# Optimization experiments

Measured on AMD Instinct MI355X. Metric: run time of the kernel, lower is better.

The kernel has to match this reference:

```python
import jax, jax.numpy as jnp
import numpy as np

SCALING = 2.0  # alpha / r = 128 / 64


def setup_inputs() -> dict:
    key = jax.random.key(0)
    k1, k2, k3, k4, k5 = jax.random.split(key, 5)
    B, S, DIN, DOUT, R = 4, 2048, 4096, 4096, 64
    x = jax.random.normal(k1, (B, S, DIN), dtype=jnp.float32)
    # int8 quantized weight codes in [-127, 127] (stored as int32 for portability)
    qweight = jax.random.randint(k2, (DOUT, DIN), -127, 128, dtype=jnp.int32)
    # per-output-row absmax dequant scale (already divided by 127)
    scale = jax.random.uniform(k3, (DOUT, 1), dtype=jnp.float32, minval=0.005, maxval=0.02)
    lora_A = jax.random.normal(k4, (R, DIN), dtype=jnp.float32) * 0.02
    lora_B = jax.random.normal(k5, (DOUT, R), dtype=jnp.float32) * 0.02
    return {"x": x, "qweight": qweight, "scale": scale, "lora_A": lora_A, "lora_B": lora_B}


def reference(x, qweight, scale, lora_A, lora_B):
    # inline int8 dequant: w[o,i] = code[o,i] * scale[o]
    w = qweight.astype(x.dtype) * scale  # [DOUT, DIN]
    base = jnp.einsum('bsi,oi->bso', x, w)
    # low-rank LoRA path: (x @ A^T) @ B^T, scaled
    xa = jnp.einsum('bsi,ri->bsr', x, lora_A)       # [B,S,R]
    lora = jnp.einsum('bsr,or->bso', xa, lora_B)    # [B,S,DOUT]
    return base + SCALING * lora
```

## Files before the change

### kernel.cpp

```cpp
#include <hip/hip_runtime.h>
#include <hip/hip_bf16.h>
#include <stdint.h>


typedef __bf16 bf16x8 __attribute__((ext_vector_type(8)));
typedef float f32x4 __attribute__((ext_vector_type(4)));
typedef int i32x4 __attribute__((ext_vector_type(4)));

#define DIN   4096
#define DOUT  4096
#define MTOT  8192
#define RNK   64
#define NT    64

__device__ inline void gload_lds16(const void* g, void* l) {
  __builtin_amdgcn_global_load_lds((const __attribute__((address_space(1))) void*)g,
                                   (__attribute__((address_space(3))) void*)l,
                                   16, 0, 0);
}

__global__ __launch_bounds__(256) void quant_x_kernel(const float* __restrict__ x,
                                                      signed char* __restrict__ Xi8,
                                                      float* __restrict__ tstep) {
  const int row = blockIdx.x, t = threadIdx.x;
  const float4* xr = (const float4*)(x + (size_t)row * DIN);
  float4 v[4];
  float m = 0.f;
#pragma unroll
  for (int s = 0; s < 4; ++s) {
    v[s] = xr[t + s * 256];
    m = fmaxf(m, fmaxf(fmaxf(fabsf(v[s].x), fabsf(v[s].y)),
                       fmaxf(fabsf(v[s].z), fabsf(v[s].w))));
  }
#pragma unroll
  for (int off = 32; off > 0; off >>= 1) m = fmaxf(m, __shfl_xor(m, off));
  __shared__ float wm[4];
  if ((t & 63) == 0) wm[t >> 6] = m;
  __syncthreads();
  m = fmaxf(fmaxf(wm[0], wm[1]), fmaxf(wm[2], wm[3]));
  m = fmaxf(m, 1e-30f);
  const float rs = 127.0f / m;
  int* orow = (int*)(Xi8 + (size_t)row * DIN);
#pragma unroll
  for (int s = 0; s < 4; ++s) {
    float e[4] = {v[s].x, v[s].y, v[s].z, v[s].w};
    union { signed char c[4]; int i; } p;
#pragma unroll
    for (int j = 0; j < 4; ++j) {
      int q = __float2int_rn(e[j] * rs);
      q = q > 127 ? 127 : (q < -127 ? -127 : q);
      p.c[j] = (signed char)q;
    }
    orow[t + s * 256] = p.i;
  }
  if (t == 0) tstep[row] = m * (1.0f / 127.0f);
}

__global__ void cvt_w_kernel(const int* __restrict__ q, signed char* __restrict__ Wi8) {
  int i = blockIdx.x * blockDim.x + threadIdx.x;
  int4 v = ((const int4*)q)[i];
  union { signed char c[4]; int i; } p;
  p.c[0] = (signed char)v.x; p.c[1] = (signed char)v.y;
  p.c[2] = (signed char)v.z; p.c[3] = (signed char)v.w;
  ((int*)Wi8)[i] = p.i;
}

__global__ __launch_bounds__(256) void cvt_ab_kernel(const float* __restrict__ A,
                                                     const float* __restrict__ B,
                                                     signed char* __restrict__ Ai8,
                                                     float* __restrict__ astep,
                                                     __bf16* __restrict__ Blt) {
  const int t = threadIdx.x;
  if (blockIdx.x < 64) {
    const int row = blockIdx.x;
    const float4* ar = (const float4*)(A + (size_t)row * DIN);
    float4 v[4];
    float m = 0.f;
#pragma unroll
    for (int s = 0; s < 4; ++s) {
      v[s] = ar[t + s * 256];
      m = fmaxf(m, fmaxf(fmaxf(fabsf(v[s].x), fabsf(v[s].y)),
                         fmaxf(fabsf(v[s].z), fabsf(v[s].w))));
    }
#pragma unroll
    for (int off = 32; off > 0; off >>= 1) m = fmaxf(m, __shfl_xor(m, off));
    __shared__ float wm[4];
    if ((t & 63) == 0) wm[t >> 6] = m;
    __syncthreads();
    m = fmaxf(fmaxf(wm[0], wm[1]), fmaxf(wm[2], wm[3]));
    m = fmaxf(m, 1e-30f);
    const float rs = 127.0f / m;
    int* orow = (int*)(Ai8 + (size_t)row * DIN);
#pragma unroll
    for (int s = 0; s < 4; ++s) {
      float e[4] = {v[s].x, v[s].y, v[s].z, v[s].w};
      union { signed char c[4]; int i; } p;
#pragma unroll
      for (int j = 0; j < 4; ++j) {
        int q = __float2int_rn(e[j] * rs);
        q = q > 127 ? 127 : (q < -127 ? -127 : q);
        p.c[j] = (signed char)q;
      }
      orow[t + s * 256] = p.i;
    }
    if (t == 0) astep[row] = m * (1.0f / 127.0f);
  } else {
    int i = (blockIdx.x - 64) * 256 + t;
    float4 v = ((const float4*)B)[i];
    union { __bf16 h[4]; uint64_t u; } p;
    p.h[0] = (__bf16)(2.0f * v.x); p.h[1] = (__bf16)(2.0f * v.y);
    p.h[2] = (__bf16)(2.0f * v.z); p.h[3] = (__bf16)(2.0f * v.w);
    ((uint64_t*)Blt)[i] = p.u;
  }
}

__global__ __launch_bounds__(128) void lora_xa_kernel(const signed char* __restrict__ Xi8,
                                                      const float* __restrict__ tstep,
                                                      const signed char* __restrict__ Ai8,
                                                      const float* __restrict__ astep,
                                                      __bf16* __restrict__ xa) {
  int wid = threadIdx.x >> 6, lane = threadIdx.x & 63;
  int rowbase = blockIdx.x * 32 + wid * 16;
  i32x4 acc[4] = {};
  const signed char* xrow = Xi8 + (size_t)(rowbase + (lane & 15)) * DIN + (lane >> 4) * 16;
  const signed char* ab = Ai8 + (size_t)(lane & 15) * DIN + (lane >> 4) * 16;
  for (int k0 = 0; k0 < DIN; k0 += 64) {
    i32x4 af = *(const i32x4*)(xrow + k0);
#pragma unroll
    for (int ni = 0; ni < 4; ++ni) {
      i32x4 bv = *(const i32x4*)(ab + (size_t)ni * 16 * DIN + k0);
      acc[ni] = __builtin_amdgcn_mfma_i32_16x16x64_i8(af, bv, acc[ni], 0, 0, 0);
    }
  }
  f32x4 tm = *(const f32x4*)&tstep[rowbase + (lane >> 4) * 4];
#pragma unroll
  for (int ni = 0; ni < 4; ++ni) {
    const int col = ni * 16 + (lane & 15);
    const float as = astep[col];
#pragma unroll
    for (int j = 0; j < 4; ++j) {
      int row = rowbase + (lane >> 4) * 4 + j;
      xa[(size_t)row * RNK + col] = (__bf16)((float)acc[ni][j] * tm[j] * as);
    }
  }
}

__global__ __launch_bounds__(512, 1) void gemm_i8_kernel(const signed char* __restrict__ Xi8,
                                                         const signed char* __restrict__ Wi8,
                                                         const float* __restrict__ scale,
                                                         const float* __restrict__ tstep,
                                                         const __bf16* __restrict__ xa,
                                                         const __bf16* __restrict__ Blt,
                                                         float* __restrict__ out) {
  extern __shared__ char smem[];
  const int tid = threadIdx.x;
  const int lane = tid & 63;
  const int w = tid >> 6;
  const int wr = w >> 2;
  const int wc = w & 3;

  const int swz = (blockIdx.x & 7) * 64 + (blockIdx.x >> 3);
  const int bx = swz & 15;
  const int by = swz >> 4;
  const size_t bm = (size_t)by * 256, bn = (size_t)bx * 256;

  const int rc = ((lane >> 4) ^ ((lane >> 1) & 3)) << 4;
  const int srow = tid >> 2;
  const int scol = ((tid & 3) ^ ((tid >> 3) & 3)) << 4;

  auto SH = [&](const signed char* g, size_t r0, int srct, int ldsoff) {
    gload_lds16(g + (r0 + srow) * (size_t)4096 + srct * 64 + scol,
                smem + ldsoff + tid * 16);
  };
  auto stage = [&](int srct, int buf) {
    int b = buf * 32768;
    SH(Xi8, bm, srct, b); SH(Xi8, bm + 128, srct, b + 8192);
    SH(Wi8, bn, srct, b + 16384); SH(Wi8, bn + 128, srct, b + 24576);
  };

  i32x4 aP[4], bP[4], aQ[4], bQ[4], a2[4];
  i32x4 acc[8][4] = {};

  stage(0, 0); stage(1, 1); stage(2, 2);
  asm volatile("s_waitcnt vmcnt(4)" ::: "memory");
  __builtin_amdgcn_s_barrier();
  {
    const int ab0 = wr * 8192 + (lane & 15) * 64 + rc;
    const int bb0 = 16384 + (wc >> 1) * 8192 + (wc & 1) * 4096 + (lane & 15) * 64 + rc;
#pragma unroll
    for (int mi = 0; mi < 4; ++mi) aP[mi] = *(const i32x4*)(smem + ab0 + mi * 1024);
#pragma unroll
    for (int ni = 0; ni < 4; ++ni) bP[ni] = *(const i32x4*)(smem + bb0 + ni * 1024);
  }

  auto body = [&](int kt, auto& ac, auto& bc, auto& an, auto& bn) {
    const int bufb = (kt & 3) * 32768;
    const int ab = bufb + wr * 8192 + (lane & 15) * 64 + rc;
    const int bb = bufb + 16384 + (wc >> 1) * 8192 + (wc & 1) * 4096 + (lane & 15) * 64 + rc;
    const int st = (kt + 3 < NT) ? kt + 3 : NT - 1;
    stage(st, (kt + 3) & 3);
#pragma unroll
    for (int mi = 0; mi < 4; ++mi)
      a2[mi] = *(const i32x4*)(smem + ab + 4096 + mi * 1024);
    __builtin_amdgcn_s_setprio(1);
#pragma unroll
    for (int mi = 0; mi < 4; ++mi)
#pragma unroll
      for (int ni = 0; ni < 4; ++ni)
        acc[mi][ni] = __builtin_amdgcn_mfma_i32_16x16x64_i8(ac[mi], bc[ni], acc[mi][ni], 0, 0, 0);
    __builtin_amdgcn_s_setprio(0);
    const int nbufb = ((kt + 1) & 3) * 32768;
    const int nab = nbufb + wr * 8192 + (lane & 15) * 64 + rc;
    const int nbb = nbufb + 16384 + (wc >> 1) * 8192 + (wc & 1) * 4096 + (lane & 15) * 64 + rc;
#pragma unroll
    for (int mi = 0; mi < 4; ++mi) an[mi] = *(const i32x4*)(smem + nab + mi * 1024);
#pragma unroll
    for (int ni = 0; ni < 4; ++ni) bn[ni] = *(const i32x4*)(smem + nbb + ni * 1024);
    __builtin_amdgcn_s_setprio(1);
#pragma unroll
    for (int mi = 0; mi < 4; ++mi)
#pragma unroll
      for (int ni = 0; ni < 4; ++ni)
        acc[4 + mi][ni] = __builtin_amdgcn_mfma_i32_16x16x64_i8(a2[mi], bc[ni], acc[4 + mi][ni], 0, 0, 0);
    __builtin_amdgcn_s_setprio(0);
    __builtin_amdgcn_sched_barrier(0);
    asm volatile("s_waitcnt vmcnt(4)" ::: "memory");
    __builtin_amdgcn_s_barrier();
  };

  for (int kt = 0; kt < NT; kt += 2) {
    body(kt, aP, bP, aQ, bQ);
    body(kt + 1, aQ, bQ, aP, bP);
  }

  const int sl_row = lane >> 3;
  const int sl_col = ((lane & 7) ^ (lane >> 3)) << 4;
  auto SBF = [&](const __bf16* g, size_t r0, int ldsoff) {
    char* d0 = smem + ldsoff + w * 2048 + lane * 16;
#pragma unroll
    for (int s = 0; s < 2; ++s) {
      const int rl = (w * 2 + s) * 8 + sl_row;
      gload_lds16((const char*)g + (r0 + rl) * 128 + sl_col, d0 + s * 1024);
    }
  };
  SBF(xa, bm, 0); SBF(xa, bm + 128, 16384);
  SBF(Blt, bn, 32768); SBF(Blt, bn + 128, 49152);

  float sc[4];
#pragma unroll
  for (int ni = 0; ni < 4; ++ni)
    sc[ni] = scale[bn + wc * 64 + ni * 16 + (lane & 15)];
  f32x4 tm[8];
#pragma unroll
  for (int mi = 0; mi < 8; ++mi)
    tm[mi] = *(const f32x4*)&tstep[bm + wr * 128 + mi * 16 + (lane >> 4) * 4];

  asm volatile("s_waitcnt vmcnt(0)" ::: "memory");
  __builtin_amdgcn_s_barrier();

  const int cx0 = ((lane >> 4) << 4) ^ ((lane & 7) << 4);
  const int cx1 = (64 | ((lane >> 4) << 4)) ^ ((lane & 7) << 4);
  const int abE = wr * 16384 + (lane & 15) * 128;
  const int bbE = 32768 + (wc >> 1) * 16384 + ((wc & 1) * 64 + (lane & 15)) * 128;

  bf16x8 bl0[4], bl1[4];
#pragma unroll
  for (int ni = 0; ni < 4; ++ni) {
    bl0[ni] = *(const bf16x8*)(smem + bbE + ni * 2048 + cx0);
    bl1[ni] = *(const bf16x8*)(smem + bbE + ni * 2048 + cx1);
  }
#pragma unroll
  for (int mi = 0; mi < 8; ++mi) {
    bf16x8 ax0 = *(const bf16x8*)(smem + abE + mi * 2048 + cx0);
    bf16x8 ax1 = *(const bf16x8*)(smem + abE + mi * 2048 + cx1);
    const size_t row = bm + wr * 128 + mi * 16 + (lane >> 4) * 4;
#pragma unroll
    for (int ni = 0; ni < 4; ++ni) {
      f32x4 l = {0.f, 0.f, 0.f, 0.f};
      l = __builtin_amdgcn_mfma_f32_16x16x32_bf16(ax0, bl0[ni], l, 0, 0, 0);
      l = __builtin_amdgcn_mfma_f32_16x16x32_bf16(ax1, bl1[ni], l, 0, 0, 0);
      const size_t col = bn + wc * 64 + ni * 16 + (lane & 15);
#pragma unroll
      for (int j = 0; j < 4; ++j)
        out[(row + j) * DOUT + col] = (float)acc[mi][ni][j] * (sc[ni] * tm[mi][j]) + l[j];
    }
  }
}

extern "C" void kernel_launch(void* const* d_in, const int* in_sizes, int n_in,
                              void* d_out, int out_size, void* d_ws, size_t ws_size,
                              hipStream_t stream) {
  const float* x = (const float*)d_in[0];
  const int* qw = (const int*)d_in[1];
  const float* scale = (const float*)d_in[2];
  const float* lA = (const float*)d_in[3];
  const float* lB = (const float*)d_in[4];
  float* out = (float*)d_out;

  char* ws = (char*)d_ws;
  signed char* Xi8 = (signed char*)ws;
  signed char* Wi8 = (signed char*)(ws + 33554432);
  __bf16* xa    = (__bf16*)(ws + 50331648);
  signed char* Ai8 = (signed char*)(ws + 51380224);
  __bf16* Blt   = (__bf16*)(ws + 51904512);
  float* tstep  = (float*)(ws + 52428800);
  float* astep  = (float*)(ws + 52461568);

  hipFuncSetAttribute((const void*)gemm_i8_kernel,
                      hipFuncAttributeMaxDynamicSharedMemorySize, 131072);

  quant_x_kernel<<<MTOT, 256, 0, stream>>>(x, Xi8, tstep);
  cvt_w_kernel<<<DOUT * (DIN / 4) / 256, 256, 0, stream>>>(qw, Wi8);
  cvt_ab_kernel<<<320, 256, 0, stream>>>(lA, lB, Ai8, astep, Blt);
  lora_xa_kernel<<<MTOT / 32, 128, 0, stream>>>(Xi8, tstep, Ai8, astep, xa);
  gemm_i8_kernel<<<(MTOT / 256) * (DOUT / 256), 512, 131072, stream>>>(
      Xi8, Wi8, scale, tstep, xa, Blt, out);
}
```

Measured before the change: 212.2 us.

## Shrink int8 GEMM tile to 128x256 with triple buffering for higher occupancy

The int8 GEMM block tile drops from 256x256 to 128x256, with 4x4 accumulators per wave instead of 8x4. The LDS pipeline moves from 4 stages of 32KB to 3 stages of 24KB, and launch bounds now allow several blocks per CU. The aim is better latency hiding through more resident blocks and twice as many blocks. The cost is lower arithmetic intensity per block, which means more global traffic for W, and the register double-buffering of fragments is gone.

```diff
diff --git a/kernel.cpp b/kernel.cpp
--- a/kernel.cpp
+++ b/kernel.cpp
@@ -12,6 +12,7 @@
 #define MTOT  8192
 #define RNK   64
 #define NT    64
+#define BUFB  24576
 
 __device__ inline void gload_lds16(const void* g, void* l) {
   __builtin_amdgcn_global_load_lds((const __attribute__((address_space(1))) void*)g,
@@ -145,7 +146,7 @@
   }
 }
 
-__global__ __launch_bounds__(512, 1) void gemm_i8_kernel(const signed char* __restrict__ Xi8,
+__global__ __launch_bounds__(512, 4) void gemm_i8_kernel(const signed char* __restrict__ Xi8,
                                                          const signed char* __restrict__ Wi8,
                                                          const float* __restrict__ scale,
                                                          const float* __restrict__ tstep,
@@ -159,10 +160,10 @@
   const int wr = w >> 2;
   const int wc = w & 3;
 
-  const int swz = (blockIdx.x & 7) * 64 + (blockIdx.x >> 3);
+  const int swz = (blockIdx.x & 7) * 128 + (blockIdx.x >> 3);
   const int bx = swz & 15;
   const int by = swz >> 4;
-  const size_t bm = (size_t)by * 256, bn = (size_t)bx * 256;
+  const size_t bm = (size_t)by * 128, bn = (size_t)bx * 256;
 
   const int rc = ((lane >> 4) ^ ((lane >> 1) & 3)) << 4;
   const int srow = tid >> 2;
@@ -173,64 +174,47 @@
                 smem + ldsoff + tid * 16);
   };
   auto stage = [&](int srct, int buf) {
-    int b = buf * 32768;
-    SH(Xi8, bm, srct, b); SH(Xi8, bm + 128, srct, b + 8192);
-    SH(Wi8, bn, srct, b + 16384); SH(Wi8, bn + 128, srct, b + 24576);
+    int b = buf * BUFB;
+    SH(Xi8, bm, srct, b);
+    SH(Wi8, bn, srct, b + 8192);
+    SH(Wi8, bn + 128, srct, b + 16384);
   };
 
-  i32x4 aP[4], bP[4], aQ[4], bQ[4], a2[4];
-  i32x4 acc[8][4] = {};
-
-  stage(0, 0); stage(1, 1); stage(2, 2);
-  asm volatile("s_waitcnt vmcnt(4)" ::: "memory");
+  const int aoff = (wr * 64 + (lane & 15)) * 64 + rc;
+  const int boff = 8192 + (wc * 64 + (lane & 15)) * 64 + rc;
+
+  i32x4 a[4], b[4];
+  i32x4 acc[4][4] = {};
+
+  stage(0, 0); stage(1, 1);
+  asm volatile("s_waitcnt vmcnt(3)" ::: "memory");
   __builtin_amdgcn_s_barrier();
-  {
-    const int ab0 = wr * 8192 + (lane & 15) * 64 + rc;
-    const int bb0 = 16384 + (wc >> 1) * 8192 + (wc & 1) * 4096 + (lane & 15) * 64 + rc;
-#pragma unroll
-    for (int mi = 0; mi < 4; ++mi) aP[mi] = *(const i32x4*)(smem + ab0 + mi * 1024);
-#pragma unroll
-    for (int ni = 0; ni < 4; ++ni) bP[ni] = *(const i32x4*)(smem + bb0 + ni * 1024);
-  }
-
-  auto body = [&](int kt, auto& ac, auto& bc, auto& an, auto& bn) {
-    const int bufb = (kt & 3) * 32768;
-    const int ab = bufb + wr * 8192 + (lane & 15) * 64 + rc;
-    const int bb = bufb + 16384 + (wc >> 1) * 8192 + (wc & 1) * 4096 + (lane & 15) * 64 + rc;
-    const int st = (kt + 3 < NT) ? kt + 3 : NT - 1;
-    stage(st, (kt + 3) & 3);
+
+  int cur = 0;
+  for (int kt = 0; kt < NT; ++kt) {
+    const int bufb = cur * BUFB;
+    if (kt < NT - 2) {
+      int sb = cur + 2; if (sb >= 3) sb -= 3;
+      stage(kt + 2, sb);
+    }
 #pragma unroll
     for (int mi = 0; mi < 4; ++mi)
-      a2[mi] = *(const i32x4*)(smem + ab + 4096 + mi * 1024);
+      a[mi] = *(const i32x4*)(smem + bufb + aoff + mi * 1024);
+#pragma unroll
+    for (int ni = 0; ni < 4; ++ni)
+      b[ni] = *(const i32x4*)(smem + bufb + boff + ni * 1024);
     __builtin_amdgcn_s_setprio(1);
 #pragma unroll
     for (int mi = 0; mi < 4; ++mi)
 #pragma unroll
       for (int ni = 0; ni < 4; ++ni)
-        acc[mi][ni] = __builtin_amdgcn_mfma_i32_16x16x64_i8(ac[mi], bc[ni], acc[mi][ni], 0, 0, 0);
-    __builtin_amdgcn_s_setprio(0);
-    const int nbufb = ((kt + 1) & 3) * 32768;
-    const int nab = nbufb + wr * 8192 + (lane & 15) * 64 + rc;
-    const int nbb = nbufb + 16384 + (wc >> 1) * 8192 + (wc & 1) * 4096 + (lane & 15) * 64 + rc;
-#pragma unroll
-    for (int mi = 0; mi < 4; ++mi) an[mi] = *(const i32x4*)(smem + nab + mi * 1024);
-#pragma unroll
-    for (int ni = 0; ni < 4; ++ni) bn[ni] = *(const i32x4*)(smem + nbb + ni * 1024);
-    __builtin_amdgcn_s_setprio(1);
-#pragma unroll
-    for (int mi = 0; mi < 4; ++mi)
-#pragma unroll
-      for (int ni = 0; ni < 4; ++ni)
-        acc[4 + mi][ni] = __builtin_amdgcn_mfma_i32_16x16x64_i8(a2[mi], bc[ni], acc[4 + mi][ni], 0, 0, 0);
+        acc[mi][ni] = __builtin_amdgcn_mfma_i32_16x16x64_i8(a[mi], b[ni], acc[mi][ni], 0, 0, 0);
     __builtin_amdgcn_s_setprio(0);
     __builtin_amdgcn_sched_barrier(0);
-    asm volatile("s_waitcnt vmcnt(4)" ::: "memory");
+    if (kt < NT - 2) { asm volatile("s_waitcnt vmcnt(3)" ::: "memory"); }
+    else if (kt == NT - 2) { asm volatile("s_waitcnt vmcnt(0)" ::: "memory"); }
     __builtin_amdgcn_s_barrier();
-  };
-
-  for (int kt = 0; kt < NT; kt += 2) {
-    body(kt, aP, bP, aQ, bQ);
-    body(kt + 1, aQ, bQ, aP, bP);
+    ++cur; if (cur >= 3) cur = 0;
   }
 
   const int sl_row = lane >> 3;
@@ -243,46 +227,39 @@
       gload_lds16((const char*)g + (r0 + rl) * 128 + sl_col, d0 + s * 1024);
     }
   };
-  SBF(xa, bm, 0); SBF(xa, bm + 128, 16384);
-  SBF(Blt, bn, 32768); SBF(Blt, bn + 128, 49152);
+  SBF(xa, bm, 0);
+  SBF(Blt, bn, 16384); SBF(Blt, bn + 128, 32768);
 
   float sc[4];
 #pragma unroll
   for (int ni = 0; ni < 4; ++ni)
     sc[ni] = scale[bn + wc * 64 + ni * 16 + (lane & 15)];
-  f32x4 tm[8];
-#pragma unroll
-  for (int mi = 0; mi < 8; ++mi)
-    tm[mi] = *(const f32x4*)&tstep[bm + wr * 128 + mi * 16 + (lane >> 4) * 4];
 
   asm volatile("s_waitcnt vmcnt(0)" ::: "memory");
   __builtin_amdgcn_s_barrier();
 
   const int cx0 = ((lane >> 4) << 4) ^ ((lane & 7) << 4);
   const int cx1 = (64 | ((lane >> 4) << 4)) ^ ((lane & 7) << 4);
-  const int abE = wr * 16384 + (lane & 15) * 128;
-  const int bbE = 32768 + (wc >> 1) * 16384 + ((wc & 1) * 64 + (lane & 15)) * 128;
-
-  bf16x8 bl0[4], bl1[4];
-#pragma unroll
-  for (int ni = 0; ni < 4; ++ni) {
-    bl0[ni] = *(const bf16x8*)(smem + bbE + ni * 2048 + cx0);
-    bl1[ni] = *(const bf16x8*)(smem + bbE + ni * 2048 + cx1);
-  }
-#pragma unroll
-  for (int mi = 0; mi < 8; ++mi) {
-    bf16x8 ax0 = *(const bf16x8*)(smem + abE + mi * 2048 + cx0);
-    bf16x8 ax1 = *(const bf16x8*)(smem + abE + mi * 2048 + cx1);
-    const size_t row = bm + wr * 128 + mi * 16 + (lane >> 4) * 4;
+  const int bltbase = 16384 + (wc >> 1) * 16384 + ((wc & 1) * 64 + (lane & 15)) * 128;
+
+#pragma unroll
+  for (int mi = 0; mi < 4; ++mi) {
+    const int axb = (wr * 64 + mi * 16 + (lane & 15)) * 128;
+    bf16x8 ax0 = *(const bf16x8*)(smem + axb + cx0);
+    bf16x8 ax1 = *(const bf16x8*)(smem + axb + cx1);
+    const size_t row = bm + wr * 64 + mi * 16 + (lane >> 4) * 4;
+    f32x4 tm = *(const f32x4*)&tstep[row];
 #pragma unroll
     for (int ni = 0; ni < 4; ++ni) {
+      bf16x8 bl0 = *(const bf16x8*)(smem + bltbase + ni * 2048 + cx0);
+      bf16x8 bl1 = *(const bf16x8*)(smem + bltbase + ni * 2048 + cx1);
       f32x4 l = {0.f, 0.f, 0.f, 0.f};
-      l = __builtin_amdgcn_mfma_f32_16x16x32_bf16(ax0, bl0[ni], l, 0, 0, 0);
-      l = __builtin_amdgcn_mfma_f32_16x16x32_bf16(ax1, bl1[ni], l, 0, 0, 0);
+      l = __builtin_amdgcn_mfma_f32_16x16x32_bf16(ax0, bl0, l, 0, 0, 0);
+      l = __builtin_amdgcn_mfma_f32_16x16x32_bf16(ax1, bl1, l, 0, 0, 0);
       const size_t col = bn + wc * 64 + ni * 16 + (lane & 15);
 #pragma unroll
       for (int j = 0; j < 4; ++j)
-        out[(row + j) * DOUT + col] = (float)acc[mi][ni][j] * (sc[ni] * tm[mi][j]) + l[j];
+        out[(row + j) * DOUT + col] = (float)acc[mi][ni][j] * (sc[ni] * tm[j]) + l[j];
     }
   }
 }
@@ -307,12 +284,12 @@
   float* astep  = (float*)(ws + 52461568);
 
   hipFuncSetAttribute((const void*)gemm_i8_kernel,
-                      hipFuncAttributeMaxDynamicSharedMemorySize, 131072);
+                      hipFuncAttributeMaxDynamicSharedMemorySize, 3 * BUFB);
 
   quant_x_kernel<<<MTOT, 256, 0, stream>>>(x, Xi8, tstep);
   cvt_w_kernel<<<DOUT * (DIN / 4) / 256, 256, 0, stream>>>(qw, Wi8);
   cvt_ab_kernel<<<320, 256, 0, stream>>>(lA, lB, Ai8, astep, Blt);
   lora_xa_kernel<<<MTOT / 32, 128, 0, stream>>>(Xi8, tstep, Ai8, astep, xa);
-  gemm_i8_kernel<<<(MTOT / 256) * (DOUT / 256), 512, 131072, stream>>>(
+  gemm_i8_kernel<<<(MTOT / 128) * (DOUT / 256), 512, 3 * BUFB, stream>>>(
       Xi8, Wi8, scale, tstep, xa, Blt, out);
 }
```

Result: slower. 222.8 us (+5.0%).
